# Kernel tuning notes

Hardware: AMD Instinct MI355X
Metric: run time of the kernel (lower is better)

The kernel has to match this reference:

```python
import jax, jax.numpy as jnp
import numpy as np

NUM_HEADS = 16
HEAD_SIZE = 64
LN_EPS = 1e-5


def setup_inputs() -> dict:
    key = jax.random.key(0)
    k1, k2, k3 = jax.random.split(key, 3)
    b, l, hidden = 2, 2048, 1024
    qkv_out = HEAD_SIZE * NUM_HEADS + 2 * HEAD_SIZE  # 1152
    x = jax.random.normal(k1, (b, l, hidden), dtype=jnp.float32)
    Wqkv = jax.random.normal(k2, (qkv_out, hidden), dtype=jnp.float32) * 0.02
    gamma = jnp.ones((qkv_out,), dtype=jnp.float32)
    beta = jnp.zeros((qkv_out,), dtype=jnp.float32)
    Wfc = jax.random.normal(k3, (hidden, HEAD_SIZE * NUM_HEADS), dtype=jnp.float32) * 0.02
    return {"x": x, "Wqkv": Wqkv, "gamma": gamma, "beta": beta, "Wfc": Wfc}


def reference(x, Wqkv, gamma, beta, Wfc):
    h, d = NUM_HEADS, HEAD_SIZE
    b, l, _ = x.shape
    # fused QKV projection (no bias), then LayerNorm over the FULL qkv dim
    qkv = jnp.einsum('blc,oc->blo', x, Wqkv)  # (b, l, (h+2)*d)
    mu = jnp.mean(qkv, axis=-1, keepdims=True)
    var = jnp.var(qkv, axis=-1, keepdims=True)
    qkv = (qkv - mu) * jax.lax.rsqrt(var + LN_EPS) * gamma + beta
    qkv = qkv.reshape(b, l, h + 2, d)
    k = qkv[:, :, 0, :]       # (b, l, d) shared K head
    v = qkv[:, :, 1, :]       # (b, l, d) shared V head
    q = qkv[:, :, 2:, :]      # (b, l, h, d) query heads
    scale = 1.0 / np.sqrt(d).astype(np.float32)
    scores = jnp.einsum('bqhd,bkd->bhqk', q, k) * scale  # (b, h, l, l)
    causal = jnp.tril(jnp.ones((l, l), dtype=bool))
    scores = jnp.where(causal, scores, jnp.finfo(scores.dtype).min)
    attn = jax.nn.softmax(scores, axis=-1)
    out = jnp.einsum('bhqk,bkd->bqhd', attn, v).reshape(b, l, h * d)
    return jnp.einsum('blo,ho->blh', out, Wfc)
```

## Files before the change

kernel.cpp:

```cpp
#include <hip/hip_runtime.h>
#include <stdint.h>

typedef __attribute__((ext_vector_type(8))) short s16x8;
typedef __attribute__((ext_vector_type(4))) float f32x4;

#define MFMA16(a, b, c) __builtin_amdgcn_mfma_f32_16x16x32_bf16((a), (b), (c), 0, 0, 0)

__device__ __forceinline__ unsigned short f2bf(float f) {
    unsigned int u = __float_as_uint(f);
    return (unsigned short)((u + 0x7FFFu + ((u >> 16) & 1u)) >> 16);
}
__device__ __forceinline__ float bf2f(unsigned short h) {
    return __uint_as_float(((unsigned int)h) << 16);
}
__device__ __forceinline__ void cvt8(unsigned short* dst, const float* src) {
    const float4 f0 = *(const float4*)(src);
    const float4 f1 = *(const float4*)(src + 4);
    s16x8 v;
    v[0] = (short)f2bf(f0.x); v[1] = (short)f2bf(f0.y);
    v[2] = (short)f2bf(f0.z); v[3] = (short)f2bf(f0.w);
    v[4] = (short)f2bf(f1.x); v[5] = (short)f2bf(f1.y);
    v[6] = (short)f2bf(f1.z); v[7] = (short)f2bf(f1.w);
    *(s16x8*)dst = v;
}
__device__ __forceinline__ void gl_lds16(const unsigned short* g, unsigned short* l) {
    __builtin_amdgcn_global_load_lds(
        (const __attribute__((address_space(1))) unsigned int*)g,
        (__attribute__((address_space(3))) unsigned int*)l,
        16, 0, 0);
}

__global__ __launch_bounds__(256) void cvt_all(const float* __restrict__ x,
                                               const float* __restrict__ wq,
                                               const float* __restrict__ wf,
                                               unsigned short* __restrict__ xb,
                                               unsigned short* __restrict__ wqb,
                                               unsigned short* __restrict__ wfb) {
    const int blk = blockIdx.x;
    const float* src;
    unsigned short* dst;
    int base;
    if (blk < 2048)      { src = x;  dst = xb;  base = blk; }
    else if (blk < 2624) { src = wq; dst = wqb; base = blk - 2048; }
    else                 { src = wf; dst = wfb; base = blk - 2624; }
    const int i = (base * 256 + threadIdx.x) * 8;
    cvt8(&dst[i], &src[i]);
}

template <bool OUT_F32>
__global__ __launch_bounds__(512, 6) void gemm_mn(const unsigned short* __restrict__ A,
                                                  const unsigned short* __restrict__ Bw,
                                                  void* __restrict__ Cout, int K, int N) {
    const int wg = blockIdx.x;
    const int xcd = wg & 7, j = wg >> 3;
    const int bm = (xcd << 2) + (j & 3);
    const int bn = j >> 2;
    const int t = threadIdx.x;
    const int lane = t & 63, w = t >> 6;
    const int quad = lane >> 4, col = lane & 15;
    const int wm = (w >> 1) * 32, wn = (w & 1) * 32;

    __shared__ alignas(16) unsigned short As[2][128 * 64];
    __shared__ alignas(16) unsigned short Bs[2][64 * 64];

    f32x4 acc[2][2];
#pragma unroll
    for (int i = 0; i < 2; ++i)
#pragma unroll
        for (int j2 = 0; j2 < 2; ++j2) acc[i][j2] = (f32x4){0.f, 0.f, 0.f, 0.f};

    const int lrow = lane >> 3;
    const int lcol = ((lane & 7) ^ lrow) * 8;
    const unsigned short* Ap = A + (size_t)(bm * 128 + w * 16 + lrow) * K + lcol;
    const unsigned short* Bp = Bw + (size_t)(bn * 64 + w * 8 + lrow) * K + lcol;

#pragma unroll
    for (int j2 = 0; j2 < 2; ++j2)
        gl_lds16(Ap + (size_t)(j2 * 8) * K, &As[0][(w * 16 + j2 * 8) * 64]);
    gl_lds16(Bp, &Bs[0][(w * 8) * 64]);
    __syncthreads();

    const int c7 = col & 7;
    const int fs0 = ((0 * 4 + quad) ^ c7) * 8;
    const int fs1 = ((1 * 4 + quad) ^ c7) * 8;

    for (int k0 = 0; k0 < K; k0 += 64) {
        const int p = (k0 >> 6) & 1;
        if (k0 + 64 < K) {
#pragma unroll
            for (int j2 = 0; j2 < 2; ++j2)
                gl_lds16(Ap + (size_t)(j2 * 8) * K + k0 + 64, &As[p ^ 1][(w * 16 + j2 * 8) * 64]);
            gl_lds16(Bp + k0 + 64, &Bs[p ^ 1][(w * 8) * 64]);
        }
        s16x8 af[2][2], bfr[2][2];
#pragma unroll
        for (int s = 0; s < 2; ++s) {
            const int fs = s ? fs1 : fs0;
#pragma unroll
            for (int i = 0; i < 2; ++i)
                af[s][i] = *(const s16x8*)&As[p][(wm + i * 16 + col) * 64 + fs];
#pragma unroll
            for (int j2 = 0; j2 < 2; ++j2)
                bfr[s][j2] = *(const s16x8*)&Bs[p][(wn + j2 * 16 + col) * 64 + fs];
        }
#pragma unroll
        for (int s = 0; s < 2; ++s)
#pragma unroll
            for (int i = 0; i < 2; ++i)
#pragma unroll
                for (int j2 = 0; j2 < 2; ++j2)
                    acc[i][j2] = MFMA16(af[s][i], bfr[s][j2], acc[i][j2]);
        __syncthreads();
    }
    const int rowb = bm * 128 + wm + quad * 4;
    const int colb = bn * 64 + wn + col;
#pragma unroll
    for (int i = 0; i < 2; ++i)
#pragma unroll
        for (int j2 = 0; j2 < 2; ++j2)
#pragma unroll
            for (int r = 0; r < 4; ++r) {
                size_t off = (size_t)(rowb + i * 16 + r) * N + colb + j2 * 16;
                if (OUT_F32) ((float*)Cout)[off] = acc[i][j2][r];
                else ((unsigned short*)Cout)[off] = f2bf(acc[i][j2][r]);
            }
}

__global__ __launch_bounds__(64) void ln_row(unsigned short* __restrict__ qkvn,
                                             const float* __restrict__ gamma,
                                             const float* __restrict__ beta,
                                             unsigned short* __restrict__ vT) {
    const int row = blockIdx.x;
    const int b = row >> 11, l = row & 2047;
    unsigned short* rp = qkvn + (size_t)row * 1152;
    const int lane = threadIdx.x;

    s16x8 v0 = *(const s16x8*)&rp[lane * 8];
    s16x8 v1 = *(const s16x8*)&rp[512 + lane * 8];
    unsigned int v2u = *(const unsigned int*)&rp[1024 + lane * 2];

    float f0[8], f1[8], f2[2];
    float s = 0.f, s2 = 0.f;
#pragma unroll
    for (int e = 0; e < 8; ++e) {
        f0[e] = bf2f((unsigned short)v0[e]);
        f1[e] = bf2f((unsigned short)v1[e]);
        s += f0[e] + f1[e];
        s2 += f0[e] * f0[e] + f1[e] * f1[e];
    }
    f2[0] = bf2f((unsigned short)(v2u & 0xFFFF));
    f2[1] = bf2f((unsigned short)(v2u >> 16));
    s += f2[0] + f2[1];
    s2 += f2[0] * f2[0] + f2[1] * f2[1];

#pragma unroll
    for (int off = 1; off < 64; off <<= 1) {
        s += __shfl_xor(s, off);
        s2 += __shfl_xor(s2, off);
    }
    const float mu = s * (1.0f / 1152.0f);
    float var = s2 * (1.0f / 1152.0f) - mu * mu;
    var = fmaxf(var, 0.0f);
    const float rstd = rsqrtf(var + 1e-5f);

    {
        s16x8 o;
#pragma unroll
        for (int e = 0; e < 8; ++e)
            o[e] = (short)f2bf((f0[e] - mu) * rstd * gamma[lane * 8 + e] + beta[lane * 8 + e]);
        *(s16x8*)&rp[lane * 8] = o;
        if (lane >= 8 && lane < 16) {
            const int d0 = lane * 8 - 64;
#pragma unroll
            for (int e = 0; e < 8; ++e)
                vT[((size_t)(b * 64 + d0 + e)) * 2048 + l] = (unsigned short)o[e];
        }
    }
    {
        s16x8 o;
#pragma unroll
        for (int e = 0; e < 8; ++e)
            o[e] = (short)f2bf((f1[e] - mu) * rstd * gamma[512 + lane * 8 + e] + beta[512 + lane * 8 + e]);
        *(s16x8*)&rp[512 + lane * 8] = o;
    }
    {
        unsigned short o0 = f2bf((f2[0] - mu) * rstd * gamma[1024 + lane * 2] + beta[1024 + lane * 2]);
        unsigned short o1 = f2bf((f2[1] - mu) * rstd * gamma[1025 + lane * 2] + beta[1025 + lane * 2]);
        *(unsigned int*)&rp[1024 + lane * 2] = ((unsigned int)o1 << 16) | o0;
    }
}

__global__ __launch_bounds__(512, 4) void attn_kernel(const unsigned short* __restrict__ qkvn,
                                                      const unsigned short* __restrict__ vT,
                                                      unsigned short* __restrict__ obuf) {
    const int b = blockIdx.x >> 3, hp = blockIdx.x & 7;
    const int yy = blockIdx.y;
    const int qb = (yy < 16) ? (31 - yy) : (yy - 16);
    const int t = threadIdx.x;
    const int lane = t & 63, w = t >> 6;
    const int quad = lane >> 4, col = lane & 15;
    const int hl = w >> 2;
    const int qhalf = (w >> 1) & 1;
    const int kpar = w & 1;

    __shared__ alignas(16) unsigned char SM[53248];
    unsigned short* Ks0 = (unsigned short*)SM;
    unsigned short* Vt0 = (unsigned short*)(SM + 16384);
    unsigned short* Qs  = (unsigned short*)(SM + 32768);
    unsigned short* Ps  = (unsigned short*)(SM + 32768) + w * 1280;

    const int srow = t >> 3;
    const int schunk = t & 7;
    const int ldsoff = srow * 64 + (schunk ^ (srow & 7)) * 8;

#pragma unroll
    for (int hh = 0; hh < 2; ++hh) {
        const unsigned short* qsrc =
            qkvn + (size_t)(b * 2048 + qb * 64 + srow) * 1152 + 128 + (hp * 2 + hh) * 64 + schunk * 8;
        s16x8 v = *(const s16x8*)qsrc;
#pragma unroll
        for (int e = 0; e < 8; ++e)
            v[e] = (short)f2bf(bf2f((unsigned short)v[e]) * 0.125f);
        *(s16x8*)&Qs[(hh * 64 + srow) * 80 + schunk * 8] = v;
    }
    __syncthreads();
    s16x8 qfr[2][2];
#pragma unroll
    for (int qf = 0; qf < 2; ++qf)
#pragma unroll
        for (int dh = 0; dh < 2; ++dh)
            qfr[qf][dh] = *(const s16x8*)&Qs[(hl * 64 + qhalf * 32 + qf * 16 + col) * 80 + dh * 32 + quad * 8];

    const unsigned short* kbase = qkvn + (size_t)(b * 2048 + srow) * 1152 + schunk * 8;
    const unsigned short* vbase = vT + (size_t)(b * 64 + srow) * 2048 + schunk * 8;
    *(uint4*)&Ks0[ldsoff] = *(const uint4*)(kbase);
    *(uint4*)&Vt0[ldsoff] = *(const uint4*)(vbase);
    __syncthreads();

    const int c7 = col & 7;
    const int koff0 = (kpar * 32 + col) * 128 + ((quad ^ c7) * 16);
    const int koff1 = (kpar * 32 + col) * 128 + (((4 + quad) ^ c7) * 16);
    const int voff = col * 128 + (((kpar * 4 + quad) ^ c7) * 16);

    f32x4 Oacc[4][2];
    float psum[2] = {0.f, 0.f};
#pragma unroll
    for (int ds = 0; ds < 4; ++ds)
#pragma unroll
        for (int qf = 0; qf < 2; ++qf) Oacc[ds][qf] = (f32x4){0.f, 0.f, 0.f, 0.f};

    const int qbase = qb * 64 + qhalf * 32;

    for (int kb = 0; kb <= qb; ++kb) {
        const int p = kb & 1;
        uint4 kreg, vreg;
        if (kb < qb) {
            kreg = *(const uint4*)(kbase + (size_t)(kb + 1) * 64 * 1152);
            vreg = *(const uint4*)(vbase + (kb + 1) * 64);
        }
        const bool diag = (kb == qb);
        if (!(diag && kpar == 1 && qhalf == 0)) {
            const bool needmask = diag && (kpar == qhalf);
            const char* kb8 = (const char*)(Ks0 + p * 4096);
            const char* vb8 = (const char*)(Vt0 + p * 4096);

#pragma unroll
            for (int nt = 0; nt < 2; ++nt) {
                const s16x8 kf0 = *(const s16x8*)(kb8 + nt * 2048 + koff0);
                const s16x8 kf1 = *(const s16x8*)(kb8 + nt * 2048 + koff1);
#pragma unroll
                for (int qf = 0; qf < 2; ++qf) {
                    f32x4 z = (f32x4){-12.f, -12.f, -12.f, -12.f};
                    z = MFMA16(kf0, qfr[qf][0], z);
                    z = MFMA16(kf1, qfr[qf][1], z);
                    const int qg = qbase + qf * 16 + col;
                    const int kl = kb * 64 + kpar * 32 + nt * 16 + quad * 4;
                    float ev[4];
#pragma unroll
                    for (int r = 0; r < 4; ++r) {
                        float sv = z[r];
                        if (needmask && (kl + r > qg)) sv = -1e30f;
                        ev[r] = __expf(sv);
                    }
                    psum[qf] += (ev[0] + ev[1]) + (ev[2] + ev[3]);
                    unsigned int plo, phi;
                    asm("v_cvt_pk_bf16_f32 %0, %1, %2" : "=v"(plo) : "v"(ev[0]), "v"(ev[1]));
                    asm("v_cvt_pk_bf16_f32 %0, %1, %2" : "=v"(phi) : "v"(ev[2]), "v"(ev[3]));
                    uint2 pk2;
                    pk2.x = plo; pk2.y = phi;
                    *(uint2*)&Ps[(qf * 16 + col) * 40 + nt * 16 + quad * 4] = pk2;
                }
            }

            const s16x8 pf0 = *(const s16x8*)&Ps[col * 40 + quad * 8];
            const s16x8 pf1 = *(const s16x8*)&Ps[(16 + col) * 40 + quad * 8];
            __builtin_amdgcn_s_setprio(1);
#pragma unroll
            for (int ds = 0; ds < 4; ++ds) {
                const s16x8 vf = *(const s16x8*)(vb8 + ds * 2048 + voff);
                Oacc[ds][0] = MFMA16(vf, pf0, Oacc[ds][0]);
                Oacc[ds][1] = MFMA16(vf, pf1, Oacc[ds][1]);
            }
            __builtin_amdgcn_s_setprio(0);
        }

        if (kb < qb) {
            *(uint4*)&Ks0[(p ^ 1) * 4096 + ldsoff] = kreg;
            *(uint4*)&Vt0[(p ^ 1) * 4096 + ldsoff] = vreg;
        }
        __syncthreads();
    }

#pragma unroll
    for (int qf = 0; qf < 2; ++qf) {
        psum[qf] += __shfl_xor(psum[qf], 16);
        psum[qf] += __shfl_xor(psum[qf], 32);
    }

    float* mg = (float*)SM + (hl * 2 + qhalf) * 2112;
    float* lm = (float*)(SM + 33792) + (hl * 2 + qhalf) * 32;
    if (kpar) {
#pragma unroll
        for (int ds = 0; ds < 4; ++ds)
#pragma unroll
            for (int qf = 0; qf < 2; ++qf)
#pragma unroll
                for (int r = 0; r < 4; ++r)
                    mg[(ds * 16 + quad * 4 + r) * 33 + qf * 16 + col] = Oacc[ds][qf][r];
        if (quad == 0) { lm[col] = psum[0]; lm[16 + col] = psum[1]; }
    }
    __syncthreads();
    if (!kpar) {
        const int h = hp * 2 + hl;
#pragma unroll
        for (int qf = 0; qf < 2; ++qf) {
            const int qglob = qbase + qf * 16 + col;
            const float inv = 1.0f / (psum[qf] + lm[qf * 16 + col]);
            const size_t base = (((size_t)b * 2048 + qglob) * 16 + h) * 64 + quad * 4;
#pragma unroll
            for (int ds = 0; ds < 4; ++ds) {
                ushort4 ov;
                unsigned short* op = (unsigned short*)&ov;
#pragma unroll
                for (int r = 0; r < 4; ++r)
                    op[r] = f2bf((Oacc[ds][qf][r] + mg[(ds * 16 + quad * 4 + r) * 33 + qf * 16 + col]) * inv);
                *(ushort4*)&obuf[base + ds * 16] = ov;
            }
        }
    }
}

extern "C" void kernel_launch(void* const* d_in, const int* in_sizes, int n_in,
                              void* d_out, int out_size, void* d_ws, size_t ws_size,
                              hipStream_t stream) {
    (void)in_sizes; (void)n_in; (void)out_size; (void)ws_size;
    const float* x     = (const float*)d_in[0];
    const float* Wqkv  = (const float*)d_in[1];
    const float* gamma = (const float*)d_in[2];
    const float* beta  = (const float*)d_in[3];
    const float* Wfc   = (const float*)d_in[4];
    float* out = (float*)d_out;

    char* ws = (char*)d_ws;
    unsigned short* xb   = (unsigned short*)ws;
    unsigned short* Wqb  = (unsigned short*)(ws + 8388608);
    unsigned short* Wfb  = (unsigned short*)(ws + 10747904);
    unsigned short* qkvn = (unsigned short*)(ws + 12845056);
    unsigned short* vT   = (unsigned short*)(ws + 22282240);
    unsigned short* abuf = (unsigned short*)ws;

    cvt_all<<<dim3(3136), 256, 0, stream>>>(x, Wqkv, Wfc, xb, Wqb, Wfb);
    gemm_mn<false><<<dim3(576), 512, 0, stream>>>(xb, Wqb, qkvn, 1024, 1152);
    ln_row<<<dim3(4096), 64, 0, stream>>>(qkvn, gamma, beta, vT);
    attn_kernel<<<dim3(16, 32), 512, 0, stream>>>(qkvn, vT, abuf);
    gemm_mn<true><<<dim3(512), 512, 0, stream>>>(abuf, Wfb, out, 1024, 1024);
}
```

Measured before the change: 145.8 us.

## Fuse LayerNorm into QKV GEMM via last-block-per-row-stripe atomic ticket

Removes the separate ln_row kernel launch. Each QKV GEMM block increments a per-row-stripe counter after writing its tile, and the block that finishes last for a 128-row stripe applies LayerNorm to those rows and writes the transposed V. Counters are zeroed inside the conversion kernel. This saves a launch and one pass over qkv, but it serialises the LN work onto a few tail blocks and removes the occupancy hint from launch_bounds.

```diff
diff --git a/kernel.cpp b/kernel.cpp
--- a/kernel.cpp
+++ b/kernel.cpp
@@ -35,8 +35,10 @@
                                                const float* __restrict__ wf,
                                                unsigned short* __restrict__ xb,
                                                unsigned short* __restrict__ wqb,
-                                               unsigned short* __restrict__ wfb) {
+                                               unsigned short* __restrict__ wfb,
+                                               unsigned int* __restrict__ cnt) {
     const int blk = blockIdx.x;
+    if (blk == 0 && threadIdx.x < 64) cnt[threadIdx.x] = 0;
     const float* src;
     unsigned short* dst;
     int base;
@@ -47,10 +49,14 @@
     cvt8(&dst[i], &src[i]);
 }
 
-template <bool OUT_F32>
-__global__ __launch_bounds__(512, 6) void gemm_mn(const unsigned short* __restrict__ A,
-                                                  const unsigned short* __restrict__ Bw,
-                                                  void* __restrict__ Cout, int K, int N) {
+template <bool OUT_F32, bool DO_LN>
+__global__ __launch_bounds__(512) void gemm_mn(const unsigned short* __restrict__ A,
+                                               const unsigned short* __restrict__ Bw,
+                                               void* __restrict__ Cout, int K, int N,
+                                               const float* __restrict__ gamma,
+                                               const float* __restrict__ beta,
+                                               unsigned short* __restrict__ vT,
+                                               unsigned int* __restrict__ cnt) {
     const int wg = blockIdx.x;
     const int xcd = wg & 7, j = wg >> 3;
     const int bm = (xcd << 2) + (j & 3);
@@ -124,69 +130,74 @@
                 if (OUT_F32) ((float*)Cout)[off] = acc[i][j2][r];
                 else ((unsigned short*)Cout)[off] = f2bf(acc[i][j2][r]);
             }
-}
-
-__global__ __launch_bounds__(64) void ln_row(unsigned short* __restrict__ qkvn,
-                                             const float* __restrict__ gamma,
-                                             const float* __restrict__ beta,
-                                             unsigned short* __restrict__ vT) {
-    const int row = blockIdx.x;
-    const int b = row >> 11, l = row & 2047;
-    unsigned short* rp = qkvn + (size_t)row * 1152;
-    const int lane = threadIdx.x;
-
-    s16x8 v0 = *(const s16x8*)&rp[lane * 8];
-    s16x8 v1 = *(const s16x8*)&rp[512 + lane * 8];
-    unsigned int v2u = *(const unsigned int*)&rp[1024 + lane * 2];
-
-    float f0[8], f1[8], f2[2];
-    float s = 0.f, s2 = 0.f;
-#pragma unroll
-    for (int e = 0; e < 8; ++e) {
-        f0[e] = bf2f((unsigned short)v0[e]);
-        f1[e] = bf2f((unsigned short)v1[e]);
-        s += f0[e] + f1[e];
-        s2 += f0[e] * f0[e] + f1[e] * f1[e];
-    }
-    f2[0] = bf2f((unsigned short)(v2u & 0xFFFF));
-    f2[1] = bf2f((unsigned short)(v2u >> 16));
-    s += f2[0] + f2[1];
-    s2 += f2[0] * f2[0] + f2[1] * f2[1];
-
-#pragma unroll
-    for (int off = 1; off < 64; off <<= 1) {
-        s += __shfl_xor(s, off);
-        s2 += __shfl_xor(s2, off);
-    }
-    const float mu = s * (1.0f / 1152.0f);
-    float var = s2 * (1.0f / 1152.0f) - mu * mu;
-    var = fmaxf(var, 0.0f);
-    const float rstd = rsqrtf(var + 1e-5f);
-
-    {
-        s16x8 o;
-#pragma unroll
-        for (int e = 0; e < 8; ++e)
-            o[e] = (short)f2bf((f0[e] - mu) * rstd * gamma[lane * 8 + e] + beta[lane * 8 + e]);
-        *(s16x8*)&rp[lane * 8] = o;
-        if (lane >= 8 && lane < 16) {
-            const int d0 = lane * 8 - 64;
-#pragma unroll
-            for (int e = 0; e < 8; ++e)
-                vT[((size_t)(b * 64 + d0 + e)) * 2048 + l] = (unsigned short)o[e];
-        }
-    }
-    {
-        s16x8 o;
-#pragma unroll
-        for (int e = 0; e < 8; ++e)
-            o[e] = (short)f2bf((f1[e] - mu) * rstd * gamma[512 + lane * 8 + e] + beta[512 + lane * 8 + e]);
-        *(s16x8*)&rp[512 + lane * 8] = o;
-    }
-    {
-        unsigned short o0 = f2bf((f2[0] - mu) * rstd * gamma[1024 + lane * 2] + beta[1024 + lane * 2]);
-        unsigned short o1 = f2bf((f2[1] - mu) * rstd * gamma[1025 + lane * 2] + beta[1025 + lane * 2]);
-        *(unsigned int*)&rp[1024 + lane * 2] = ((unsigned int)o1 << 16) | o0;
+
+    if constexpr (DO_LN) {
+        __shared__ int ticket_s;
+        __threadfence();
+        __syncthreads();
+        if (t == 0) ticket_s = (int)atomicAdd(cnt + bm, 1u);
+        __syncthreads();
+        if (ticket_s == (N >> 6) - 1) {
+            __threadfence();
+            unsigned short* qk = (unsigned short*)Cout;
+            const int wv = t >> 6, ln2 = t & 63;
+#pragma unroll 1
+            for (int ri = 0; ri < 16; ++ri) {
+                const int row = bm * 128 + wv * 16 + ri;
+                const int bb = row >> 11, ll = row & 2047;
+                unsigned short* rp = qk + (size_t)row * 1152;
+                s16x8 v0 = *(const s16x8*)&rp[ln2 * 8];
+                s16x8 v1 = *(const s16x8*)&rp[512 + ln2 * 8];
+                unsigned int v2u = *(const unsigned int*)&rp[1024 + ln2 * 2];
+                float f0[8], f1[8], f2[2];
+                float s = 0.f, s2 = 0.f;
+#pragma unroll
+                for (int e = 0; e < 8; ++e) {
+                    f0[e] = bf2f((unsigned short)v0[e]);
+                    f1[e] = bf2f((unsigned short)v1[e]);
+                    s += f0[e] + f1[e];
+                    s2 += f0[e] * f0[e] + f1[e] * f1[e];
+                }
+                f2[0] = bf2f((unsigned short)(v2u & 0xFFFF));
+                f2[1] = bf2f((unsigned short)(v2u >> 16));
+                s += f2[0] + f2[1];
+                s2 += f2[0] * f2[0] + f2[1] * f2[1];
+#pragma unroll
+                for (int off = 1; off < 64; off <<= 1) {
+                    s += __shfl_xor(s, off);
+                    s2 += __shfl_xor(s2, off);
+                }
+                const float mu = s * (1.0f / 1152.0f);
+                float var = s2 * (1.0f / 1152.0f) - mu * mu;
+                var = fmaxf(var, 0.0f);
+                const float rstd = rsqrtf(var + 1e-5f);
+                {
+                    s16x8 o;
+#pragma unroll
+                    for (int e = 0; e < 8; ++e)
+                        o[e] = (short)f2bf((f0[e] - mu) * rstd * gamma[ln2 * 8 + e] + beta[ln2 * 8 + e]);
+                    *(s16x8*)&rp[ln2 * 8] = o;
+                    if (ln2 >= 8 && ln2 < 16) {
+                        const int d0 = ln2 * 8 - 64;
+#pragma unroll
+                        for (int e = 0; e < 8; ++e)
+                            vT[((size_t)(bb * 64 + d0 + e)) * 2048 + ll] = (unsigned short)o[e];
+                    }
+                }
+                {
+                    s16x8 o;
+#pragma unroll
+                    for (int e = 0; e < 8; ++e)
+                        o[e] = (short)f2bf((f1[e] - mu) * rstd * gamma[512 + ln2 * 8 + e] + beta[512 + ln2 * 8 + e]);
+                    *(s16x8*)&rp[512 + ln2 * 8] = o;
+                }
+                {
+                    unsigned short o0 = f2bf((f2[0] - mu) * rstd * gamma[1024 + ln2 * 2] + beta[1024 + ln2 * 2]);
+                    unsigned short o1 = f2bf((f2[1] - mu) * rstd * gamma[1025 + ln2 * 2] + beta[1025 + ln2 * 2]);
+                    *(unsigned int*)&rp[1024 + ln2 * 2] = ((unsigned int)o1 << 16) | o0;
+                }
+            }
+        }
     }
 }
 
@@ -367,11 +378,13 @@
     unsigned short* Wfb  = (unsigned short*)(ws + 10747904);
     unsigned short* qkvn = (unsigned short*)(ws + 12845056);
     unsigned short* vT   = (unsigned short*)(ws + 22282240);
+    unsigned int*   cnt  = (unsigned int*)(ws + 23068672);
     unsigned short* abuf = (unsigned short*)ws;
 
-    cvt_all<<<dim3(3136), 256, 0, stream>>>(x, Wqkv, Wfc, xb, Wqb, Wfb);
-    gemm_mn<false><<<dim3(576), 512, 0, stream>>>(xb, Wqb, qkvn, 1024, 1152);
-    ln_row<<<dim3(4096), 64, 0, stream>>>(qkvn, gamma, beta, vT);
+    cvt_all<<<dim3(3136), 256, 0, stream>>>(x, Wqkv, Wfc, xb, Wqb, Wfb, cnt);
+    gemm_mn<false, true><<<dim3(576), 512, 0, stream>>>(xb, Wqb, qkvn, 1024, 1152,
+                                                        gamma, beta, vT, cnt);
     attn_kernel<<<dim3(16, 32), 512, 0, stream>>>(qkvn, vT, abuf);
-    gemm_mn<true><<<dim3(512), 512, 0, stream>>>(abuf, Wfb, out, 1024, 1024);
-}
+    gemm_mn<true, false><<<dim3(512), 512, 0, stream>>>(abuf, Wfb, out, 1024, 1024,
+                                                        nullptr, nullptr, nullptr, nullptr);
+}
```

New measurement: 302.4 us. +107.4%, slower.
